# Optimization experiments

Hardware: AMD Instinct MI355X
Metric: run time of the kernel (lower is better)

Reference implementation:

```python
import jax, jax.numpy as jnp
import numpy as np

D_MODEL, D_FF, D_NEURON, N_HEADS = 1024, 4096, 128, 8
HEAD_DIM = D_NEURON // N_HEADS
LN_EPS = 1e-5

def gelu(x):
    return jax.nn.gelu(x, approximate=False)  # torch default is exact erf GELU

def setup_inputs() -> dict:
    key = jax.random.key(0)
    ks = jax.random.split(key, 16)
    s = 0.02
    inp = {
        "x": jax.random.normal(ks[0], (2, 2048, D_MODEL), jnp.float32),
        "neuron_patterns": jax.random.normal(ks[1], (D_FF, D_MODEL), jnp.float32) * s,
        "neuron_vecs": jax.random.normal(ks[2], (D_FF, D_NEURON), jnp.float32) * s,
        "neuron_out_dirs": jax.random.normal(ks[3], (D_FF, D_MODEL), jnp.float32) * s,
        "router_w1": jax.random.normal(ks[4], (D_MODEL, D_MODEL), jnp.float32) * s,
        "router_w2": jax.random.normal(ks[5], (D_FF, D_MODEL), jnp.float32) * s,
        "ln_g": jnp.ones((D_MODEL,), jnp.float32),
        "ln_b": jnp.zeros((D_MODEL,), jnp.float32),
        "in_proj_w": jax.random.normal(ks[6], (3 * D_NEURON, D_NEURON), jnp.float32) * s,
        "in_proj_b": jnp.zeros((3 * D_NEURON,), jnp.float32),
        "out_proj_w": jax.random.normal(ks[7], (D_NEURON, D_NEURON), jnp.float32) * s,
        "out_proj_b": jnp.zeros((D_NEURON,), jnp.float32),
        "wp1_w": jax.random.normal(ks[8], (D_NEURON // 2, D_NEURON), jnp.float32) * s,
        "wp1_b": jnp.zeros((D_NEURON // 2,), jnp.float32),
        "wp2_w": jax.random.normal(ks[9], (1, D_NEURON // 2), jnp.float32) * s,
        "wp2_b": jnp.zeros((1,), jnp.float32),
        "top_k": 32,
    }
    return inp

def _forward(x, neuron_patterns, neuron_vecs, neuron_out_dirs, router_w1, router_w2,
             ln_g, ln_b, in_proj_w, in_proj_b, out_proj_w, out_proj_b,
             wp1_w, wp1_b, wp2_w, wp2_b, top_k):
    B, S, D = x.shape
    xf = x.reshape(-1, D)                                  # [N, D]
    # Router (MLP): LayerNorm -> gelu(x @ W1^T) -> @ W2^T
    mu = jnp.mean(xf, axis=-1, keepdims=True)
    var = jnp.mean(jnp.square(xf - mu), axis=-1, keepdims=True)
    xn = (xf - mu) * jax.lax.rsqrt(var + LN_EPS) * ln_g + ln_b
    h = gelu(xn @ router_w1.T)
    scores = h @ router_w2.T                               # [N, d_ff]
    _, idx = jax.lax.top_k(scores, top_k)                  # [N, k]
    pats = neuron_patterns[idx]                            # [N, k, D]
    sems = neuron_vecs[idx]                                # [N, k, dn]
    dirs = neuron_out_dirs[idx]                            # [N, k, D]
    base = gelu(jnp.einsum('nd,nkd->nk', xf, pats))        # [N, k]
    # Small self-attention over the k gathered neuron semantics (eval: no dropout)
    qkv = sems @ in_proj_w.T + in_proj_b                   # [N, k, 3*dn]
    q, kk, v = jnp.split(qkv, 3, axis=-1)
    N, K = q.shape[0], q.shape[1]
    q = q.reshape(N, K, N_HEADS, HEAD_DIM)
    kk = kk.reshape(N, K, N_HEADS, HEAD_DIM)
    v = v.reshape(N, K, N_HEADS, HEAD_DIM)
    att = jnp.einsum('nqhd,nkhd->nhqk', q, kk) / jnp.sqrt(jnp.float32(HEAD_DIM))
    att = jax.nn.softmax(att, axis=-1)
    ao = jnp.einsum('nhqk,nkhd->nqhd', att, v).reshape(N, K, D_NEURON)
    attended = ao @ out_proj_w.T + out_proj_b              # [N, k, dn]
    # Gate: sigmoid(MLP(attended)) -> [N, k, 1]
    sw = jax.nn.sigmoid(gelu(attended @ wp1_w.T + wp1_b) @ wp2_w.T + wp2_b)
    final = base[..., None] * sw                           # [N, k, 1]
    out = jnp.einsum('nko,nkd->nd', final, dirs)           # sum over k neurons
    return out.reshape(B, S, D)

def reference(x, neuron_patterns, neuron_vecs, neuron_out_dirs, router_w1, router_w2,
              ln_g, ln_b, in_proj_w, in_proj_b, out_proj_w, out_proj_b,
              wp1_w, wp1_b, wp2_w, wp2_b, top_k):
    return _forward(x, neuron_patterns, neuron_vecs, neuron_out_dirs, router_w1, router_w2,
                    ln_g, ln_b, in_proj_w, in_proj_b, out_proj_w, out_proj_b,
                    wp1_w, wp1_b, wp2_w, wp2_b, top_k)
```

## Files before the change

### kernel.cpp

```cpp
#include <hip/hip_runtime.h>
#include <math.h>

#define N_TOK 4096
#define DM 1024
#define DFF 4096
#define DN 128
#define NH 8
#define HD 16
#define KSEL 32
#define KCAND 48
#define KMAX 64

typedef __attribute__((ext_vector_type(4))) float floatx4;
typedef __attribute__((ext_vector_type(8))) short short8;
typedef __attribute__((ext_vector_type(8))) unsigned short ushort8v;
typedef __attribute__((ext_vector_type(4))) unsigned short ushort4v;

__device__ __forceinline__ float gelu_f(float x) {
  return 0.5f * x * (1.0f + erff(x * 0.70710678118654752440f));
}
__device__ __forceinline__ float bf2f(unsigned short u) {
  union { unsigned int i; float f; } v; v.i = ((unsigned int)u) << 16; return v.f;
}
__device__ __forceinline__ unsigned short f2bf(float f) {
  unsigned int x = __float_as_uint(f);
  unsigned int r = (x + 0x7fffu + ((x >> 16) & 1u)) >> 16;
  return (unsigned short)r;
}
__device__ __forceinline__ void split3(float v, unsigned short& h, unsigned short& m,
                                       unsigned short& lo) {
  h = f2bf(v);
  float r1 = v - bf2f(h);
  m = f2bf(r1);
  float r2 = r1 - bf2f(m);
  lo = f2bf(r2);
}

__global__ __launch_bounds__(256) void ln3_kernel(const float* __restrict__ x,
    const float* __restrict__ g, const float* __restrict__ b,
    unsigned short* __restrict__ xh, unsigned short* __restrict__ xm,
    unsigned short* __restrict__ xl) {
  int n = blockIdx.x, tid = threadIdx.x;
  const float* row = x + (size_t)n * DM;
  float s = 0.f, sq = 0.f;
  for (int i = tid; i < DM; i += 256) { float v = row[i]; s += v; sq += v * v; }
  for (int off = 32; off; off >>= 1) { s += __shfl_down(s, off); sq += __shfl_down(sq, off); }
  __shared__ float ss[4], ssq[4];
  __shared__ float s_mu, s_rs;
  int wid = tid >> 6;
  if ((tid & 63) == 0) { ss[wid] = s; ssq[wid] = sq; }
  __syncthreads();
  if (tid == 0) {
    float S = ss[0] + ss[1] + ss[2] + ss[3];
    float Q = ssq[0] + ssq[1] + ssq[2] + ssq[3];
    float mu = S * (1.f / DM);
    float var = Q * (1.f / DM) - mu * mu;
    s_mu = mu; s_rs = rsqrtf(var + 1e-5f);
  }
  __syncthreads();
  float mu = s_mu, rs = s_rs;
  size_t base = (size_t)n * DM;
  for (int i = tid; i < DM; i += 256) {
    float v = (row[i] - mu) * rs * g[i] + b[i];
    unsigned short h, m, lo;
    split3(v, h, m, lo);
    xh[base + i] = h; xm[base + i] = m; xl[base + i] = lo;
  }
}

__global__ __launch_bounds__(256) void cvt_split3(const float* __restrict__ in,
    unsigned short* __restrict__ oh, unsigned short* __restrict__ om,
    unsigned short* __restrict__ ol) {
  int i = (blockIdx.x * 256 + threadIdx.x) * 4;
  float4 v = *(const float4*)(in + i);
  unsigned short h0, m0, l0, h1, m1, l1, h2, m2, l2, h3, m3, l3;
  split3(v.x, h0, m0, l0);
  split3(v.y, h1, m1, l1);
  split3(v.z, h2, m2, l2);
  split3(v.w, h3, m3, l3);
  ushort4v hh = {h0, h1, h2, h3};
  ushort4v mm = {m0, m1, m2, m3};
  ushort4v ll = {l0, l1, l2, l3};
  *(ushort4v*)(oh + i) = hh;
  *(ushort4v*)(om + i) = mm;
  *(ushort4v*)(ol + i) = ll;
}

__global__ __launch_bounds__(256) void cvt_bf16(const float* __restrict__ in,
    unsigned short* __restrict__ out) {
  int i = (blockIdx.x * 256 + threadIdx.x) * 4;
  float4 v = *(const float4*)(in + i);
  ushort4v o = {f2bf(v.x), f2bf(v.y), f2bf(v.z), f2bf(v.w)};
  *(ushort4v*)(out + i) = o;
}

__global__ __launch_bounds__(256, 1) void gemm1s(
    const unsigned short* __restrict__ Ah_, const unsigned short* __restrict__ Am_,
    const unsigned short* __restrict__ Al_, const unsigned short* __restrict__ Bh_,
    const unsigned short* __restrict__ Bm_, const unsigned short* __restrict__ Bl_,
    float* __restrict__ H, unsigned short* __restrict__ Hb) {
  __shared__ short Ahs[128 * 32], Ams[128 * 32], Als[128 * 32];
  __shared__ short Bhs[128 * 32], Bms[128 * 32], Bls[128 * 32];
  const int K = 1024;
  const int N = DM;
  int tid = threadIdx.x;
  int w = tid >> 6, l = tid & 63;
  size_t brow = (size_t)blockIdx.y * 128;
  size_t bcol = (size_t)blockIdx.x * 128;

  int r0 = w * 32 + (l >> 2);
  int g0 = (l & 3) ^ ((r0 >> 1) & 3);
  size_t oA0 = (brow + r0) * (size_t)K + g0 * 8;
  size_t oA1 = (brow + r0 + 16) * (size_t)K + g0 * 8;
  size_t oB0 = (bcol + r0) * (size_t)K + g0 * 8;
  size_t oB1 = (bcol + r0 + 16) * (size_t)K + g0 * 8;
  const short* gAh0 = (const short*)Ah_ + oA0; const short* gAh1 = (const short*)Ah_ + oA1;
  const short* gAm0 = (const short*)Am_ + oA0; const short* gAm1 = (const short*)Am_ + oA1;
  const short* gAl0 = (const short*)Al_ + oA0; const short* gAl1 = (const short*)Al_ + oA1;
  const short* gBh0 = (const short*)Bh_ + oB0; const short* gBh1 = (const short*)Bh_ + oB1;
  const short* gBm0 = (const short*)Bm_ + oB0; const short* gBm1 = (const short*)Bm_ + oB1;
  const short* gBl0 = (const short*)Bl_ + oB0; const short* gBl1 = (const short*)Bl_ + oB1;
  short* lAh = &Ahs[w * 1024]; short* lAm = &Ams[w * 1024]; short* lAl = &Als[w * 1024];
  short* lBh = &Bhs[w * 1024]; short* lBm = &Bms[w * 1024]; short* lBl = &Bls[w * 1024];

  const short8 *pah[4], *pam[4], *pal[4], *pbh[4], *pbm[4], *pbl[4];
#pragma unroll
  for (int i = 0; i < 4; i++) {
    int m = (w >> 1) * 64 + i * 16 + (l & 15);
    int slot = m * 4 + ((l >> 4) ^ ((m >> 1) & 3));
    pah[i] = (const short8*)&Ahs[slot * 8];
    pam[i] = (const short8*)&Ams[slot * 8];
    pal[i] = (const short8*)&Als[slot * 8];
    int nn = (w & 1) * 64 + i * 16 + (l & 15);
    int slotb = nn * 4 + ((l >> 4) ^ ((nn >> 1) & 3));
    pbh[i] = (const short8*)&Bhs[slotb * 8];
    pbm[i] = (const short8*)&Bms[slotb * 8];
    pbl[i] = (const short8*)&Bls[slotb * 8];
  }

  floatx4 acc[4][4];
#pragma unroll
  for (int i = 0; i < 4; i++)
#pragma unroll
    for (int j = 0; j < 4; j++) acc[i][j] = (floatx4){0.f, 0.f, 0.f, 0.f};

#define GLD(GP, LB) \
  __builtin_amdgcn_global_load_lds((const __attribute__((address_space(1))) unsigned int*)(GP), \
                                   (__attribute__((address_space(3))) unsigned int*)(LB), 16, 0, 0)

  for (int k0 = 0; k0 < K; k0 += 32) {
    __syncthreads();
    GLD(gAh0 + k0, lAh); GLD(gAh1 + k0, lAh + 512);
    GLD(gAm0 + k0, lAm); GLD(gAm1 + k0, lAm + 512);
    GLD(gAl0 + k0, lAl); GLD(gAl1 + k0, lAl + 512);
    GLD(gBh0 + k0, lBh); GLD(gBh1 + k0, lBh + 512);
    GLD(gBm0 + k0, lBm); GLD(gBm1 + k0, lBm + 512);
    GLD(gBl0 + k0, lBl); GLD(gBl1 + k0, lBl + 512);
    __syncthreads();
    short8 ah[4], am[4], al[4], bh[4], bm[4], bl[4];
#pragma unroll
    for (int i = 0; i < 4; i++) {
      ah[i] = *pah[i]; am[i] = *pam[i]; al[i] = *pal[i];
      bh[i] = *pbh[i]; bm[i] = *pbm[i]; bl[i] = *pbl[i];
    }
#pragma unroll
    for (int i = 0; i < 4; i++)
#pragma unroll
      for (int j = 0; j < 4; j++)
        acc[i][j] = __builtin_amdgcn_mfma_f32_16x16x32_bf16(ah[i], bh[j], acc[i][j], 0, 0, 0);
#pragma unroll
    for (int i = 0; i < 4; i++)
#pragma unroll
      for (int j = 0; j < 4; j++)
        acc[i][j] = __builtin_amdgcn_mfma_f32_16x16x32_bf16(am[i], bh[j], acc[i][j], 0, 0, 0);
#pragma unroll
    for (int i = 0; i < 4; i++)
#pragma unroll
      for (int j = 0; j < 4; j++)
        acc[i][j] = __builtin_amdgcn_mfma_f32_16x16x32_bf16(ah[i], bm[j], acc[i][j], 0, 0, 0);
#pragma unroll
    for (int i = 0; i < 4; i++)
#pragma unroll
      for (int j = 0; j < 4; j++)
        acc[i][j] = __builtin_amdgcn_mfma_f32_16x16x32_bf16(al[i], bh[j], acc[i][j], 0, 0, 0);
#pragma unroll
    for (int i = 0; i < 4; i++)
#pragma unroll
      for (int j = 0; j < 4; j++)
        acc[i][j] = __builtin_amdgcn_mfma_f32_16x16x32_bf16(ah[i], bl[j], acc[i][j], 0, 0, 0);
#pragma unroll
    for (int i = 0; i < 4; i++)
#pragma unroll
      for (int j = 0; j < 4; j++)
        acc[i][j] = __builtin_amdgcn_mfma_f32_16x16x32_bf16(am[i], bm[j], acc[i][j], 0, 0, 0);
  }
#undef GLD

#pragma unroll
  for (int i = 0; i < 4; i++) {
#pragma unroll
    for (int j = 0; j < 4; j++) {
#pragma unroll
      for (int r = 0; r < 4; r++) {
        size_t row = brow + (w >> 1) * 64 + i * 16 + (l >> 4) * 4 + r;
        size_t col = bcol + (w & 1) * 64 + j * 16 + (l & 15);
        float v = gelu_f(acc[i][j][r]);
        H[row * N + col] = v;
        Hb[row * N + col] = f2bf(v);
      }
    }
  }
}

__global__ __launch_bounds__(256) void gemm_bf(const unsigned short* __restrict__ Ah,
    const unsigned short* __restrict__ Bh, unsigned short* __restrict__ C) {
  __shared__ short Asd[128 * 32];
  __shared__ short Bsd[128 * 32];
  const int K = 1024;
  int tid = threadIdx.x;
  int w = tid >> 6, l = tid & 63;
  size_t brow = (size_t)blockIdx.y * 128;
  size_t bcol = (size_t)blockIdx.x * 128;
  const short* Ab = (const short*)Ah + brow * K;
  const short* Bb = (const short*)Bh + bcol * K;

  int r0 = w * 32 + (l >> 2);
  int g0 = (l & 3) ^ ((r0 >> 1) & 3);
  const short* Ag0 = Ab + (size_t)r0 * K + g0 * 8;
  const short* Ag1 = Ab + (size_t)(r0 + 16) * K + g0 * 8;
  const short* Bg0 = Bb + (size_t)r0 * K + g0 * 8;
  const short* Bg1 = Bb + (size_t)(r0 + 16) * K + g0 * 8;
  short* ALds0 = &Asd[w * 1024];
  short* ALds1 = &Asd[w * 1024 + 512];
  short* BLds0 = &Bsd[w * 1024];
  short* BLds1 = &Bsd[w * 1024 + 512];

  const short8* aptr[4];
  const short8* bptr[4];
#pragma unroll
  for (int i = 0; i < 4; i++) {
    int m = (w >> 1) * 64 + i * 16 + (l & 15);
    int slot = m * 4 + ((l >> 4) ^ ((m >> 1) & 3));
    aptr[i] = (const short8*)&Asd[slot * 8];
    int n = (w & 1) * 64 + i * 16 + (l & 15);
    int slotb = n * 4 + ((l >> 4) ^ ((n >> 1) & 3));
    bptr[i] = (const short8*)&Bsd[slotb * 8];
  }

  floatx4 acc[4][4];
#pragma unroll
  for (int i = 0; i < 4; i++)
#pragma unroll
    for (int j = 0; j < 4; j++) acc[i][j] = (floatx4){0.f, 0.f, 0.f, 0.f};

  for (int k0 = 0; k0 < K; k0 += 32) {
    __syncthreads();
    __builtin_amdgcn_global_load_lds((const __attribute__((address_space(1))) unsigned int*)(Ag0 + k0),
                                     (__attribute__((address_space(3))) unsigned int*)ALds0, 16, 0, 0);
    __builtin_amdgcn_global_load_lds((const __attribute__((address_space(1))) unsigned int*)(Ag1 + k0),
                                     (__attribute__((address_space(3))) unsigned int*)ALds1, 16, 0, 0);
    __builtin_amdgcn_global_load_lds((const __attribute__((address_space(1))) unsigned int*)(Bg0 + k0),
                                     (__attribute__((address_space(3))) unsigned int*)BLds0, 16, 0, 0);
    __builtin_amdgcn_global_load_lds((const __attribute__((address_space(1))) unsigned int*)(Bg1 + k0),
                                     (__attribute__((address_space(3))) unsigned int*)BLds1, 16, 0, 0);
    __syncthreads();
    short8 a[4], b[4];
#pragma unroll
    for (int i = 0; i < 4; i++) a[i] = *aptr[i];
#pragma unroll
    for (int j = 0; j < 4; j++) b[j] = *bptr[j];
#pragma unroll
    for (int i = 0; i < 4; i++)
#pragma unroll
      for (int j = 0; j < 4; j++)
        acc[i][j] = __builtin_amdgcn_mfma_f32_16x16x32_bf16(a[i], b[j], acc[i][j], 0, 0, 0);
  }

#pragma unroll
  for (int i = 0; i < 4; i++) {
#pragma unroll
    for (int j = 0; j < 4; j++) {
#pragma unroll
      for (int r = 0; r < 4; r++) {
        size_t row = brow + (w >> 1) * 64 + i * 16 + (l >> 4) * 4 + r;
        size_t col = bcol + (w & 1) * 64 + j * 16 + (l & 15);
        C[row * DFF + col] = f2bf(acc[i][j][r]);
      }
    }
  }
}

__global__ __launch_bounds__(256) void topk2_kernel(const unsigned short* __restrict__ scores,
    int* __restrict__ cand, int* __restrict__ cnt) {
  int wv = threadIdx.x >> 6, l = threadIdx.x & 63;
  int n = blockIdx.x * 4 + wv;
  const ushort8v* row = (const ushort8v*)(scores + (size_t)n * DFF);
  unsigned short key[64];
#pragma unroll
  for (int i = 0; i < 8; i++) {
    ushort8v v = row[l * 8 + i];
#pragma unroll
    for (int e = 0; e < 8; e++) {
      unsigned short u = v[e];
      key[i * 8 + e] = (u & 0x8000u) ? (unsigned short)(~u)
                                     : (unsigned short)(u | 0x8000u);
    }
  }
  unsigned int prefix = 0;
#pragma unroll
  for (int bit = 15; bit >= 0; bit--) {
    unsigned int probe = prefix | (1u << bit);
    int c = 0;
#pragma unroll
    for (int i = 0; i < 64; i++) c += (key[i] >= probe) ? 1 : 0;
#pragma unroll
    for (int s = 1; s < 64; s <<= 1) c += __shfl_xor(c, s);
    if (c >= KCAND) prefix = probe;
  }
  unsigned short thr = (unsigned short)prefix;
  unsigned long long ltmask = (1ull << l) - 1ull;
  int base = 0;
  int* outp = cand + (size_t)n * KMAX;
#pragma unroll
  for (int i = 0; i < 64; i++) {
    bool p = key[i] >= thr;
    unsigned long long m = __ballot(p);
    if (p) {
      int pos = base + __popcll(m & ltmask);
      if (pos < KMAX) outp[pos] = l * 64 + i;
    }
    base += __popcll(m);
  }
  if (l == 0) cnt[n] = base < KMAX ? base : KMAX;
}

__global__ __launch_bounds__(256) void rescore_kernel(const float* __restrict__ h,
    const float* __restrict__ w2f, const int* __restrict__ cand,
    const int* __restrict__ cnt, int* __restrict__ idx32) {
  __shared__ float sh[DM];
  __shared__ float sc[KMAX];
  __shared__ int sidx[KMAX];
  __shared__ int s_cnt;
  int n = blockIdx.x, tid = threadIdx.x;
  *(float4*)&sh[tid * 4] = *(const float4*)(h + (size_t)n * DM + tid * 4);
  if (tid == 0) s_cnt = cnt[n];
  if (tid < KMAX) { sidx[tid] = cand[(size_t)n * KMAX + tid]; sc[tid] = -INFINITY; }
  __syncthreads();
  int cntv = s_cnt;
  int w = tid >> 6, lane = tid & 63;
  for (int c = w; c < cntv; c += 4) {
    const float4* row = (const float4*)(w2f + (size_t)sidx[c] * DM);
    const float4* hp = (const float4*)sh;
    float s = 0.f;
#pragma unroll
    for (int t = 0; t < 4; t++) {
      float4 wv = row[t * 64 + lane];
      float4 hv = hp[t * 64 + lane];
      s = fmaf(wv.x, hv.x, s); s = fmaf(wv.y, hv.y, s);
      s = fmaf(wv.z, hv.z, s); s = fmaf(wv.w, hv.w, s);
    }
    for (int off = 32; off; off >>= 1) s += __shfl_xor(s, off);
    if (lane == 0) sc[c] = s;
  }
  __syncthreads();
  if (tid < cntv) {
    float st = sc[tid]; int it = sidx[tid];
    int rank = 0;
    for (int j = 0; j < KMAX; j++) {
      float sj = sc[j];
      rank += (sj > st) || (sj == st && sidx[j] < it);
    }
    if (rank < KSEL) idx32[(size_t)n * KSEL + rank] = it;
  }
}

__global__ __launch_bounds__(384) void qkvtab_kernel(const float* __restrict__ nv,
    const float* __restrict__ ipw, const float* __restrict__ ipb,
    unsigned short* __restrict__ tab) {
  __shared__ float s_nv[8 * 128];
  int f0 = blockIdx.x * 8;
  int tid = threadIdx.x;
  for (int i = tid; i < 8 * 128; i += 384) s_nv[i] = nv[(size_t)f0 * 128 + i];
  __syncthreads();
  int row = tid;
  float bias = ipb[row];
  float acc[8];
#pragma unroll
  for (int ff = 0; ff < 8; ff++) acc[ff] = bias;
  const float* wr = ipw + (size_t)row * 128;
  for (int c = 0; c < 128; c++) {
    float w = wr[c];
#pragma unroll
    for (int ff = 0; ff < 8; ff++) acc[ff] = fmaf(s_nv[ff * 128 + c], w, acc[ff]);
  }
#pragma unroll
  for (int ff = 0; ff < 8; ff++) tab[(size_t)(f0 + ff) * 384 + row] = f2bf(acc[ff]);
}

#define AOS 132
__global__ __launch_bounds__(128) void tail3_kernel(
    const float* __restrict__ xf, const unsigned short* __restrict__ pats_b,
    const unsigned short* __restrict__ dirs_b, const unsigned short* __restrict__ qtab_b,
    const int* __restrict__ idxs,
    const unsigned short* __restrict__ opwb, const float* __restrict__ opb,
    const unsigned short* __restrict__ w1b, const float* __restrict__ b1,
    const float* __restrict__ w2, const float* __restrict__ b2,
    float* __restrict__ out) {
  __shared__ unsigned short s_kv[2 * 32 * 128];
  __shared__ unsigned short s_xf[1024];
  __shared__ unsigned short s_ao[32 * AOS];
  __shared__ float s_base[32];
  __shared__ float s_coef[32];
  __shared__ int s_idx[32];
  unsigned short* s_k = s_kv;
  unsigned short* s_v = s_kv + 32 * 128;
  unsigned short* s_at = s_kv;

  int n = blockIdx.x, tid = threadIdx.x;
  int w = tid >> 6, l = tid & 63;

  if (tid < 32) s_idx[tid] = idxs[(size_t)n * 32 + tid];
  {
    const float4* xr = (const float4*)(xf + (size_t)n * DM);
    float4 a = xr[tid * 2], b = xr[tid * 2 + 1];
    ushort8v o = {f2bf(a.x), f2bf(a.y), f2bf(a.z), f2bf(a.w),
                  f2bf(b.x), f2bf(b.y), f2bf(b.z), f2bf(b.w)};
    *(ushort8v*)&s_xf[tid * 8] = o;
  }
  __syncthreads();

#pragma unroll
  for (int p = 0; p < 8; p++) {
    int i = p * 128 + tid;
    int j = i >> 5, c = i & 31;
    int half = c >> 4, cc = c & 15;
    ushort8v v = *(const ushort8v*)(qtab_b + (size_t)s_idx[j] * 384 + 128 + half * 128 + cc * 8);
    *(ushort8v*)&s_kv[half * 4096 + j * 128 + cc * 8] = v;
  }

  {
    int j = tid >> 2, lq = tid & 3;
    const ushort8v* pr = (const ushort8v*)(pats_b + (size_t)s_idx[j] * 1024);
    float s = 0.f;
#pragma unroll 8
    for (int it = 0; it < 32; it++) {
      int g = it * 4 + lq;
      ushort8v pv = pr[g];
      const ushort8v xv = *(const ushort8v*)&s_xf[g * 8];
#pragma unroll
      for (int e = 0; e < 8; e++) s = fmaf(bf2f(pv[e]), bf2f(xv[e]), s);
    }
    s += __shfl_xor(s, 1);
    s += __shfl_xor(s, 2);
    if (lq == 0) s_base[j] = gelu_f(s);
  }
  __syncthreads();

  {
    int qj = l & 31;
#pragma unroll
    for (int p = 0; p < 2; p++) {
      int h0 = w * 4 + p * 2 + (l >> 5);
      const ushort8v* qr = (const ushort8v*)(qtab_b + (size_t)s_idx[qj] * 384 + h0 * 16);
      ushort8v q0 = qr[0], q1 = qr[1];
      float q[16];
#pragma unroll
      for (int e = 0; e < 8; e++) { q[e] = bf2f(q0[e]); q[8 + e] = bf2f(q1[e]); }
      float att[32];
#pragma unroll 8
      for (int kj = 0; kj < 32; kj++) {
        const ushort8v* kr = (const ushort8v*)&s_k[kj * 128 + h0 * 16];
        ushort8v k0 = kr[0], k1 = kr[1];
        float s = 0.f;
#pragma unroll
        for (int e = 0; e < 8; e++) s = fmaf(q[e], bf2f(k0[e]), s);
#pragma unroll
        for (int e = 0; e < 8; e++) s = fmaf(q[8 + e], bf2f(k1[e]), s);
        att[kj] = s * 0.25f;
      }
      float m = att[0];
#pragma unroll
      for (int k = 1; k < 32; k++) m = fmaxf(m, att[k]);
      float sum = 0.f;
#pragma unroll
      for (int k = 0; k < 32; k++) { att[k] = expf(att[k] - m); sum += att[k]; }
      float inv = 1.f / sum;
#pragma unroll
      for (int k = 0; k < 32; k++) att[k] *= inv;
      float o[16];
#pragma unroll
      for (int e = 0; e < 16; e++) o[e] = 0.f;
#pragma unroll 8
      for (int kj = 0; kj < 32; kj++) {
        const ushort8v* vr = (const ushort8v*)&s_v[kj * 128 + h0 * 16];
        ushort8v v0 = vr[0], v1 = vr[1];
        float a = att[kj];
#pragma unroll
        for (int e = 0; e < 8; e++) o[e] = fmaf(a, bf2f(v0[e]), o[e]);
#pragma unroll
        for (int e = 0; e < 8; e++) o[8 + e] = fmaf(a, bf2f(v1[e]), o[8 + e]);
      }
      ushort8v o0, o1;
#pragma unroll
      for (int e = 0; e < 8; e++) { o0[e] = f2bf(o[e]); o1[e] = f2bf(o[8 + e]); }
      ushort8v* ao = (ushort8v*)&s_ao[qj * AOS + h0 * 16];
      ao[0] = o0; ao[1] = o1;
    }
  }
  __syncthreads();

  {
    floatx4 acc[8];
#pragma unroll
    for (int nt = 0; nt < 8; nt++) acc[nt] = (floatx4){0.f, 0.f, 0.f, 0.f};
#pragma unroll
    for (int kst = 0; kst < 4; kst++) {
      short8 a = *(const short8*)&s_ao[(w * 16 + (l & 15)) * AOS + kst * 32 + (l >> 4) * 8];
#pragma unroll
      for (int nt = 0; nt < 8; nt++) {
        short8 b = *(const short8*)&opwb[(size_t)(nt * 16 + (l & 15)) * 128 + kst * 32 + (l >> 4) * 8];
        acc[nt] = __builtin_amdgcn_mfma_f32_16x16x32_bf16(a, b, acc[nt], 0, 0, 0);
      }
    }
#pragma unroll
    for (int nt = 0; nt < 8; nt++) {
      int col = nt * 16 + (l & 15);
      float bias = opb[col];
#pragma unroll
      for (int r = 0; r < 4; r++) {
        int row = w * 16 + (l >> 4) * 4 + r;
        s_at[row * AOS + col] = f2bf(acc[nt][r] + bias);
      }
    }
  }
  __syncthreads();

  {
    floatx4 acc[4];
#pragma unroll
    for (int nt = 0; nt < 4; nt++) acc[nt] = (floatx4){0.f, 0.f, 0.f, 0.f};
#pragma unroll
    for (int kst = 0; kst < 4; kst++) {
      short8 a = *(const short8*)&s_at[(w * 16 + (l & 15)) * AOS + kst * 32 + (l >> 4) * 8];
#pragma unroll
      for (int nt = 0; nt < 4; nt++) {
        short8 b = *(const short8*)&w1b[(size_t)(nt * 16 + (l & 15)) * 128 + kst * 32 + (l >> 4) * 8];
        acc[nt] = __builtin_amdgcn_mfma_f32_16x16x32_bf16(a, b, acc[nt], 0, 0, 0);
      }
    }
    float p[4] = {0.f, 0.f, 0.f, 0.f};
#pragma unroll
    for (int nt = 0; nt < 4; nt++) {
      int col = nt * 16 + (l & 15);
      float bb = b1[col], ww = w2[col];
#pragma unroll
      for (int r = 0; r < 4; r++)
        p[r] = fmaf(gelu_f(acc[nt][r] + bb), ww, p[r]);
    }
#pragma unroll
    for (int r = 0; r < 4; r++) {
      p[r] += __shfl_xor(p[r], 1);
      p[r] += __shfl_xor(p[r], 2);
      p[r] += __shfl_xor(p[r], 4);
      p[r] += __shfl_xor(p[r], 8);
    }
    if ((l & 15) == 0) {
      float b2v = b2[0];
#pragma unroll
      for (int r = 0; r < 4; r++) {
        int row = w * 16 + (l >> 4) * 4 + r;
        float sw = 1.f / (1.f + expf(-(p[r] + b2v)));
        s_coef[row] = s_base[row] * sw;
      }
    }
  }
  __syncthreads();

#pragma unroll
  for (int ii = 0; ii < 2; ii++) {
    int d0 = (ii * 128 + tid) * 4;
    float4 a = {0.f, 0.f, 0.f, 0.f};
#pragma unroll 8
    for (int j = 0; j < 32; j++) {
      float c = s_coef[j];
      ushort4v dv = *(const ushort4v*)&dirs_b[(size_t)s_idx[j] * 1024 + d0];
      a.x = fmaf(c, bf2f(dv.x), a.x);
      a.y = fmaf(c, bf2f(dv.y), a.y);
      a.z = fmaf(c, bf2f(dv.z), a.z);
      a.w = fmaf(c, bf2f(dv.w), a.w);
    }
    *(float4*)&out[(size_t)n * 1024 + d0] = a;
  }
}

extern "C" void kernel_launch(void* const* d_in, const int* in_sizes, int n_in,
                              void* d_out, int out_size, void* d_ws, size_t ws_size,
                              hipStream_t stream) {
  const float* x    = (const float*)d_in[0];
  const float* pats = (const float*)d_in[1];
  const float* nv   = (const float*)d_in[2];
  const float* dirs = (const float*)d_in[3];
  const float* rw1  = (const float*)d_in[4];
  const float* rw2  = (const float*)d_in[5];
  const float* lng  = (const float*)d_in[6];
  const float* lnb  = (const float*)d_in[7];
  const float* ipw  = (const float*)d_in[8];
  const float* ipb  = (const float*)d_in[9];
  const float* opw  = (const float*)d_in[10];
  const float* opb  = (const float*)d_in[11];
  const float* w1   = (const float*)d_in[12];
  const float* b1   = (const float*)d_in[13];
  const float* w2   = (const float*)d_in[14];
  const float* b2   = (const float*)d_in[15];
  float* out = (float*)d_out;

  const size_t MB = 1u << 20;
  char* ws = (char*)d_ws;
  unsigned short* xnh  = (unsigned short*)(ws + 0);
  unsigned short* xnm  = (unsigned short*)(ws + 8 * MB);
  float* h             = (float*)(ws + 16 * MB);
  unsigned short* sb   = (unsigned short*)(ws + 32 * MB);
  unsigned short* w1h  = (unsigned short*)(ws + 32 * MB);
  unsigned short* w1m  = (unsigned short*)(ws + 34 * MB);
  unsigned short* w1l  = (unsigned short*)(ws + 36 * MB);
  unsigned short* xnl  = (unsigned short*)(ws + 38 * MB);
  unsigned short* qtab = (unsigned short*)(ws + 64 * MB);
  unsigned short* hb   = (unsigned short*)(ws + 67 * MB);
  unsigned short* w2b  = (unsigned short*)(ws + 75 * MB);
  unsigned short* patsb= (unsigned short*)(ws + 83 * MB);
  unsigned short* dirsb= (unsigned short*)(ws + 91 * MB);
  unsigned short* opwb = (unsigned short*)(ws + 99 * MB);
  unsigned short* w1b  = (unsigned short*)(ws + 99 * MB + 64 * 1024);
  int* idx32           = (int*)(ws + 100 * MB);
  int* cand            = (int*)(ws + 101 * MB);
  int* cnt             = (int*)(ws + 102 * MB);

  ln3_kernel<<<N_TOK, 256, 0, stream>>>(x, lng, lnb, xnh, xnm, xnl);
  cvt_split3<<<(DM * DM) / 1024, 256, 0, stream>>>(rw1, w1h, w1m, w1l);
  gemm1s<<<dim3(DM / 128, N_TOK / 128), 256, 0, stream>>>(xnh, xnm, xnl, w1h, w1m, w1l, h, hb);
  cvt_bf16<<<(DFF * DM) / 1024, 256, 0, stream>>>(rw2, w2b);
  cvt_bf16<<<(DFF * DM) / 1024, 256, 0, stream>>>(pats, patsb);
  cvt_bf16<<<(DFF * DM) / 1024, 256, 0, stream>>>(dirs, dirsb);
  cvt_bf16<<<(DN * DN) / 1024, 256, 0, stream>>>(opw, opwb);
  cvt_bf16<<<(DN * DN / 2) / 1024, 256, 0, stream>>>(w1, w1b);
  gemm_bf<<<dim3(DFF / 128, N_TOK / 128), 256, 0, stream>>>(hb, w2b, sb);
  topk2_kernel<<<N_TOK / 4, 256, 0, stream>>>(sb, cand, cnt);
  rescore_kernel<<<N_TOK, 256, 0, stream>>>(h, rw2, cand, cnt, idx32);
  qkvtab_kernel<<<DFF / 8, 384, 0, stream>>>(nv, ipw, ipb, qtab);
  tail3_kernel<<<N_TOK, 128, 0, stream>>>(x, patsb, dirsb, qtab, idx32,
                                          opwb, opb, w1b, b1, w2, b2, out);
}
```

Before: 547.9 us.

## Read fp32 patterns and directions directly in tail, drop bf16 conversions, use 256 threads

Removes the two cvt_bf16 launches that converted the full 4096x1024 pattern and direction matrices to bf16 every call. The tail kernel now gathers fp32 rows directly for the base dot product and the output accumulation, and x is kept in fp32. The tail block grows from 128 to 256 threads, with work redistributed across attention heads and the out_proj MFMA column tiles. This saves roughly 32MB of conversion traffic and two launches, at the cost of gathering twice as many bytes per selected row in the tail and leaving two waves idle during the gate MLP.

```diff
diff --git a/kernel.cpp b/kernel.cpp
--- a/kernel.cpp
+++ b/kernel.cpp
@@ -398,16 +398,16 @@
 }
 
 #define AOS 132
-__global__ __launch_bounds__(128) void tail3_kernel(
-    const float* __restrict__ xf, const unsigned short* __restrict__ pats_b,
-    const unsigned short* __restrict__ dirs_b, const unsigned short* __restrict__ qtab_b,
+__global__ __launch_bounds__(256) void tail4_kernel(
+    const float* __restrict__ xf, const float* __restrict__ pats,
+    const float* __restrict__ dirs, const unsigned short* __restrict__ qtab_b,
     const int* __restrict__ idxs,
     const unsigned short* __restrict__ opwb, const float* __restrict__ opb,
     const unsigned short* __restrict__ w1b, const float* __restrict__ b1,
     const float* __restrict__ w2, const float* __restrict__ b2,
     float* __restrict__ out) {
   __shared__ unsigned short s_kv[2 * 32 * 128];
-  __shared__ unsigned short s_xf[1024];
+  __shared__ float s_x[1024];
   __shared__ unsigned short s_ao[32 * AOS];
   __shared__ float s_base[32];
   __shared__ float s_coef[32];
@@ -420,18 +420,12 @@
   int w = tid >> 6, l = tid & 63;
 
   if (tid < 32) s_idx[tid] = idxs[(size_t)n * 32 + tid];
-  {
-    const float4* xr = (const float4*)(xf + (size_t)n * DM);
-    float4 a = xr[tid * 2], b = xr[tid * 2 + 1];
-    ushort8v o = {f2bf(a.x), f2bf(a.y), f2bf(a.z), f2bf(a.w),
-                  f2bf(b.x), f2bf(b.y), f2bf(b.z), f2bf(b.w)};
-    *(ushort8v*)&s_xf[tid * 8] = o;
-  }
-  __syncthreads();
-
-#pragma unroll
-  for (int p = 0; p < 8; p++) {
-    int i = p * 128 + tid;
+  *(float4*)&s_x[tid * 4] = *(const float4*)(xf + (size_t)n * DM + tid * 4);
+  __syncthreads();
+
+#pragma unroll
+  for (int p = 0; p < 4; p++) {
+    int i = p * 256 + tid;
     int j = i >> 5, c = i & 31;
     int half = c >> 4, cc = c & 15;
     ushort8v v = *(const ushort8v*)(qtab_b + (size_t)s_idx[j] * 384 + 128 + half * 128 + cc * 8);
@@ -439,103 +433,103 @@
   }
 
   {
-    int j = tid >> 2, lq = tid & 3;
-    const ushort8v* pr = (const ushort8v*)(pats_b + (size_t)s_idx[j] * 1024);
+    int j = tid >> 3, g = tid & 7;
+    const float4* pr = (const float4*)(pats + (size_t)s_idx[j] * DM);
+    const float4* xp = (const float4*)s_x;
     float s = 0.f;
 #pragma unroll 8
     for (int it = 0; it < 32; it++) {
-      int g = it * 4 + lq;
-      ushort8v pv = pr[g];
-      const ushort8v xv = *(const ushort8v*)&s_xf[g * 8];
-#pragma unroll
-      for (int e = 0; e < 8; e++) s = fmaf(bf2f(pv[e]), bf2f(xv[e]), s);
+      float4 pv = pr[it * 8 + g];
+      float4 xv = xp[it * 8 + g];
+      s = fmaf(pv.x, xv.x, s); s = fmaf(pv.y, xv.y, s);
+      s = fmaf(pv.z, xv.z, s); s = fmaf(pv.w, xv.w, s);
     }
     s += __shfl_xor(s, 1);
     s += __shfl_xor(s, 2);
-    if (lq == 0) s_base[j] = gelu_f(s);
+    s += __shfl_xor(s, 4);
+    if (g == 0) s_base[j] = gelu_f(s);
   }
   __syncthreads();
 
   {
     int qj = l & 31;
-#pragma unroll
-    for (int p = 0; p < 2; p++) {
-      int h0 = w * 4 + p * 2 + (l >> 5);
-      const ushort8v* qr = (const ushort8v*)(qtab_b + (size_t)s_idx[qj] * 384 + h0 * 16);
-      ushort8v q0 = qr[0], q1 = qr[1];
-      float q[16];
-#pragma unroll
-      for (int e = 0; e < 8; e++) { q[e] = bf2f(q0[e]); q[8 + e] = bf2f(q1[e]); }
-      float att[32];
+    int h0 = w * 2 + (l >> 5);
+    const ushort8v* qr = (const ushort8v*)(qtab_b + (size_t)s_idx[qj] * 384 + h0 * 16);
+    ushort8v q0 = qr[0], q1 = qr[1];
+    float q[16];
+#pragma unroll
+    for (int e = 0; e < 8; e++) { q[e] = bf2f(q0[e]); q[8 + e] = bf2f(q1[e]); }
+    float att[32];
 #pragma unroll 8
-      for (int kj = 0; kj < 32; kj++) {
-        const ushort8v* kr = (const ushort8v*)&s_k[kj * 128 + h0 * 16];
-        ushort8v k0 = kr[0], k1 = kr[1];
-        float s = 0.f;
-#pragma unroll
-        for (int e = 0; e < 8; e++) s = fmaf(q[e], bf2f(k0[e]), s);
-#pragma unroll
-        for (int e = 0; e < 8; e++) s = fmaf(q[8 + e], bf2f(k1[e]), s);
-        att[kj] = s * 0.25f;
-      }
-      float m = att[0];
-#pragma unroll
-      for (int k = 1; k < 32; k++) m = fmaxf(m, att[k]);
-      float sum = 0.f;
-#pragma unroll
-      for (int k = 0; k < 32; k++) { att[k] = expf(att[k] - m); sum += att[k]; }
-      float inv = 1.f / sum;
-#pragma unroll
-      for (int k = 0; k < 32; k++) att[k] *= inv;
-      float o[16];
-#pragma unroll
-      for (int e = 0; e < 16; e++) o[e] = 0.f;
+    for (int kj = 0; kj < 32; kj++) {
+      const ushort8v* kr = (const ushort8v*)&s_k[kj * 128 + h0 * 16];
+      ushort8v k0 = kr[0], k1 = kr[1];
+      float s = 0.f;
+#pragma unroll
+      for (int e = 0; e < 8; e++) s = fmaf(q[e], bf2f(k0[e]), s);
+#pragma unroll
+      for (int e = 0; e < 8; e++) s = fmaf(q[8 + e], bf2f(k1[e]), s);
+      att[kj] = s * 0.25f;
+    }
+    float m = att[0];
+#pragma unroll
+    for (int k = 1; k < 32; k++) m = fmaxf(m, att[k]);
+    float sum = 0.f;
+#pragma unroll
+    for (int k = 0; k < 32; k++) { att[k] = expf(att[k] - m); sum += att[k]; }
+    float inv = 1.f / sum;
+#pragma unroll
+    for (int k = 0; k < 32; k++) att[k] *= inv;
+    float o[16];
+#pragma unroll
+    for (int e = 0; e < 16; e++) o[e] = 0.f;
 #pragma unroll 8
-      for (int kj = 0; kj < 32; kj++) {
-        const ushort8v* vr = (const ushort8v*)&s_v[kj * 128 + h0 * 16];
-        ushort8v v0 = vr[0], v1 = vr[1];
-        float a = att[kj];
-#pragma unroll
-        for (int e = 0; e < 8; e++) o[e] = fmaf(a, bf2f(v0[e]), o[e]);
-#pragma unroll
-        for (int e = 0; e < 8; e++) o[8 + e] = fmaf(a, bf2f(v1[e]), o[8 + e]);
-      }
-      ushort8v o0, o1;
-#pragma unroll
-      for (int e = 0; e < 8; e++) { o0[e] = f2bf(o[e]); o1[e] = f2bf(o[8 + e]); }
-      ushort8v* ao = (ushort8v*)&s_ao[qj * AOS + h0 * 16];
-      ao[0] = o0; ao[1] = o1;
-    }
+    for (int kj = 0; kj < 32; kj++) {
+      const ushort8v* vr = (const ushort8v*)&s_v[kj * 128 + h0 * 16];
+      ushort8v v0 = vr[0], v1 = vr[1];
+      float a = att[kj];
+#pragma unroll
+      for (int e = 0; e < 8; e++) o[e] = fmaf(a, bf2f(v0[e]), o[e]);
+#pragma unroll
+      for (int e = 0; e < 8; e++) o[8 + e] = fmaf(a, bf2f(v1[e]), o[8 + e]);
+    }
+    ushort8v o0, o1;
+#pragma unroll
+    for (int e = 0; e < 8; e++) { o0[e] = f2bf(o[e]); o1[e] = f2bf(o[8 + e]); }
+    ushort8v* ao = (ushort8v*)&s_ao[qj * AOS + h0 * 16];
+    ao[0] = o0; ao[1] = o1;
   }
   __syncthreads();
 
   {
-    floatx4 acc[8];
-#pragma unroll
-    for (int nt = 0; nt < 8; nt++) acc[nt] = (floatx4){0.f, 0.f, 0.f, 0.f};
+    floatx4 acc[4];
+#pragma unroll
+    for (int nt = 0; nt < 4; nt++) acc[nt] = (floatx4){0.f, 0.f, 0.f, 0.f};
+    int rbase = (w & 1) * 16;
+    int cblk = (w >> 1) * 4;
 #pragma unroll
     for (int kst = 0; kst < 4; kst++) {
-      short8 a = *(const short8*)&s_ao[(w * 16 + (l & 15)) * AOS + kst * 32 + (l >> 4) * 8];
-#pragma unroll
-      for (int nt = 0; nt < 8; nt++) {
-        short8 b = *(const short8*)&opwb[(size_t)(nt * 16 + (l & 15)) * 128 + kst * 32 + (l >> 4) * 8];
+      short8 a = *(const short8*)&s_ao[(rbase + (l & 15)) * AOS + kst * 32 + (l >> 4) * 8];
+#pragma unroll
+      for (int nt = 0; nt < 4; nt++) {
+        short8 b = *(const short8*)&opwb[(size_t)((cblk + nt) * 16 + (l & 15)) * 128 + kst * 32 + (l >> 4) * 8];
         acc[nt] = __builtin_amdgcn_mfma_f32_16x16x32_bf16(a, b, acc[nt], 0, 0, 0);
       }
     }
 #pragma unroll
-    for (int nt = 0; nt < 8; nt++) {
-      int col = nt * 16 + (l & 15);
+    for (int nt = 0; nt < 4; nt++) {
+      int col = (cblk + nt) * 16 + (l & 15);
       float bias = opb[col];
 #pragma unroll
       for (int r = 0; r < 4; r++) {
-        int row = w * 16 + (l >> 4) * 4 + r;
+        int row = rbase + (l >> 4) * 4 + r;
         s_at[row * AOS + col] = f2bf(acc[nt][r] + bias);
       }
     }
   }
   __syncthreads();
 
-  {
+  if (w < 2) {
     floatx4 acc[4];
 #pragma unroll
     for (int nt = 0; nt < 4; nt++) acc[nt] = (floatx4){0.f, 0.f, 0.f, 0.f};
@@ -576,18 +570,17 @@
   }
   __syncthreads();
 
-#pragma unroll
-  for (int ii = 0; ii < 2; ii++) {
-    int d0 = (ii * 128 + tid) * 4;
+  {
+    int d0 = tid * 4;
     float4 a = {0.f, 0.f, 0.f, 0.f};
 #pragma unroll 8
     for (int j = 0; j < 32; j++) {
       float c = s_coef[j];
-      ushort4v dv = *(const ushort4v*)&dirs_b[(size_t)s_idx[j] * 1024 + d0];
-      a.x = fmaf(c, bf2f(dv.x), a.x);
-      a.y = fmaf(c, bf2f(dv.y), a.y);
-      a.z = fmaf(c, bf2f(dv.z), a.z);
-      a.w = fmaf(c, bf2f(dv.w), a.w);
+      float4 dv = *(const float4*)(dirs + (size_t)s_idx[j] * DM + d0);
+      a.x = fmaf(c, dv.x, a.x);
+      a.y = fmaf(c, dv.y, a.y);
+      a.z = fmaf(c, dv.z, a.z);
+      a.w = fmaf(c, dv.w, a.w);
     }
     *(float4*)&out[(size_t)n * 1024 + d0] = a;
   }
@@ -627,8 +620,6 @@
   unsigned short* qtab = (unsigned short*)(ws + 64 * MB);
   unsigned short* hb   = (unsigned short*)(ws + 67 * MB);
   unsigned short* w2b  = (unsigned short*)(ws + 75 * MB);
-  unsigned short* patsb= (unsigned short*)(ws + 83 * MB);
-  unsigned short* dirsb= (unsigned short*)(ws + 91 * MB);
   unsigned short* opwb = (unsigned short*)(ws + 99 * MB);
   unsigned short* w1b  = (unsigned short*)(ws + 99 * MB + 64 * 1024);
   int* idx32           = (int*)(ws + 100 * MB);
@@ -639,14 +630,12 @@
   cvt_split3<<<(DM * DM) / 1024, 256, 0, stream>>>(rw1, w1h, w1m, w1l);
   gemm1s<<<dim3(DM / 128, N_TOK / 128), 256, 0, stream>>>(xnh, xnm, xnl, w1h, w1m, w1l, h, hb);
   cvt_bf16<<<(DFF * DM) / 1024, 256, 0, stream>>>(rw2, w2b);
-  cvt_bf16<<<(DFF * DM) / 1024, 256, 0, stream>>>(pats, patsb);
-  cvt_bf16<<<(DFF * DM) / 1024, 256, 0, stream>>>(dirs, dirsb);
   cvt_bf16<<<(DN * DN) / 1024, 256, 0, stream>>>(opw, opwb);
   cvt_bf16<<<(DN * DN / 2) / 1024, 256, 0, stream>>>(w1, w1b);
   gemm_bf<<<dim3(DFF / 128, N_TOK / 128), 256, 0, stream>>>(hb, w2b, sb);
   topk2_kernel<<<N_TOK / 4, 256, 0, stream>>>(sb, cand, cnt);
   rescore_kernel<<<N_TOK, 256, 0, stream>>>(h, rw2, cand, cnt, idx32);
   qkvtab_kernel<<<DFF / 8, 384, 0, stream>>>(nv, ipw, ipb, qtab);
-  tail3_kernel<<<N_TOK, 128, 0, stream>>>(x, patsb, dirsb, qtab, idx32,
+  tail4_kernel<<<N_TOK, 256, 0, stream>>>(x, pats, dirs, qtab, idx32,
                                           opwb, opb, w1b, b1, w2, b2, out);
 }
```

New measurement: 545.3 us. No clear change (-0.5%).
